# Optimization experiments

Measured on AMD Instinct MI355X. Metric: run time of the kernel, lower is better.

## Reference

```python
import jax, jax.numpy as jnp
import numpy as np

N = 100000   # num nodes
E = 3200000  # num edges (avg degree 32)
D = 256      # in_channels
H = 256      # hidden_dim
C = 1        # num_class
G = 512      # num graphs in batch


def setup_inputs() -> dict:
    key = jax.random.key(0)
    k = jax.random.split(key, 5)
    x = jax.random.normal(k[0], (N, D), dtype=jnp.float32)
    edge_index = jax.random.randint(k[1], (2, E), 0, N, dtype=jnp.int64)
    batch = jnp.sort(jax.random.randint(k[2], (N,), 0, G, dtype=jnp.int64))
    # GCNLayer.proj: Linear(D, H); model.lin: Linear(H, C)
    W1 = jax.random.normal(k[3], (H, D), dtype=jnp.float32) * 0.05
    b1 = jnp.zeros((H,), dtype=jnp.float32)
    W2 = jax.random.normal(k[4], (C, H), dtype=jnp.float32) * 0.05
    b2 = jnp.zeros((C,), dtype=jnp.float32)
    return {"x": x, "edge_index": edge_index, "batch": batch,
            "W1": W1, "b1": b1, "W2": W2, "b2": b2}


def reference(x, edge_index, batch, W1, b1, W2, b2):
    src, dst = edge_index[0], edge_index[1]
    # degree(edge_index[0]) over ORIGINAL edges (before self-loops), as in source
    deg = jnp.zeros((N,), x.dtype).at[src].add(jnp.asarray(1.0, x.dtype))
    norm = deg ** -0.5  # D^{-1/2}
    # (D^{-1/2} (A + I) D^{-1/2}) x
    # edge term: out[src] += norm[src] * norm[dst] * x[dst]
    msg = (norm[src] * norm[dst])[:, None] * x[dst]          # [E, D]
    agg = jax.ops.segment_sum(msg, src, num_segments=N)      # [N, D]
    agg = agg + (norm * norm)[:, None] * x                   # self-loop term
    h = jax.nn.relu(agg @ W1.T + b1)                          # [N, H]
    pooled = jax.ops.segment_max(h, batch, num_segments=G)   # [G, H]
    out = pooled @ W2.T + b2                                  # [G, 1]
    return jnp.squeeze(out, axis=1)                           # [G]
```

## Files before the change

kernel.cpp:

```cpp
#include <hip/hip_runtime.h>
#include <cstddef>

#define NN    100000
#define EE    3200000
#define GG    512
#define NBK2  391
#define BCAP  9216
#define TT    4096

typedef __attribute__((ext_vector_type(8))) short bf16x8;
typedef __attribute__((ext_vector_type(4))) float f32x4;
typedef __attribute__((ext_vector_type(8))) unsigned short u16x8;

struct U12 { unsigned a, b, c; };

static __device__ __forceinline__ unsigned short f2b(float f) {
  unsigned u = __float_as_uint(f);
  unsigned r = u + 0x7fffu + ((u >> 16) & 1u);
  return (unsigned short)(r >> 16);
}

__global__ __launch_bounds__(1024, 2) void k_split(const int* __restrict__ src,
                                                   const int* __restrict__ dst,
                                                   int* __restrict__ gcur,
                                                   int* __restrict__ pk) {
  __shared__ int hist[NBK2], st[NBK2], cur[NBK2], gbase[NBK2];
  __shared__ int sc[512];
  __shared__ int sorted[TT];
  __shared__ unsigned short binof[TT];
  const int tid = threadIdx.x;
  const int t0  = blockIdx.x * TT;
  const int tc  = min(TT, EE - t0);

  if (tid < NBK2) hist[tid] = 0;
  __syncthreads();
  int myk[4], myw[4];
#pragma unroll
  for (int r = 0; r < 4; ++r) {
    int j = r * 1024 + tid;
    myk[r] = -1;
    if (j < tc) {
      int s = src[t0 + j], d = dst[t0 + j];
      myk[r] = s >> 8;
      myw[r] = ((s & 255) << 17) | d;
      atomicAdd(&hist[myk[r]], 1);
    }
  }
  __syncthreads();
  if (tid < 512) sc[tid] = (tid < NBK2) ? hist[tid] : 0;
  __syncthreads();
  for (int d = 1; d < 512; d <<= 1) {
    int v = (tid < 512 && tid >= d) ? sc[tid - d] : 0;
    __syncthreads();
    if (tid < 512) sc[tid] += v;
    __syncthreads();
  }
  if (tid < NBK2) { st[tid] = tid ? sc[tid - 1] : 0; cur[tid] = st[tid]; }
  __syncthreads();
#pragma unroll
  for (int r = 0; r < 4; ++r) {
    if (myk[r] >= 0) {
      int pos = atomicAdd(&cur[myk[r]], 1);
      sorted[pos] = myw[r];
      binof[pos] = (unsigned short)myk[r];
    }
  }
  __syncthreads();
  if (tid < NBK2) {
    int c = cur[tid] - st[tid];
    gbase[tid] = c ? atomicAdd(&gcur[tid], c) : 0;
  }
  __syncthreads();
  for (int j = tid; j < tc; j += 1024) {
    int k   = binof[j];
    int idx = gbase[k] + (j - st[k]);
    if (idx < BCAP) pk[(size_t)k * BCAP + idx] = sorted[j];
  }
}

__global__ __launch_bounds__(512) void k_prep(const int* __restrict__ gcur,
                                              const int* __restrict__ pk,
                                              const float* __restrict__ x,
                                              const float* __restrict__ w1,
                                              unsigned short* __restrict__ wbf,
                                              int* __restrict__ csr,
                                              int* __restrict__ ro,
                                              int* __restrict__ xm) {
  __shared__ int hist[256], start[257], cur[256], sc[256];
  __shared__ float red[8];
  const int tid = threadIdx.x;
  const int b   = blockIdx.x;
  const int n0  = b * 256;

  if (tid < 256) hist[tid] = 0;
  __syncthreads();
  const int szc = min(gcur[b], BCAP);
  const int* __restrict__ pb = pk + (size_t)b * BCAP;
  for (int j = tid; j < szc; j += 512)
    atomicAdd(&hist[pb[j] >> 17], 1);
  __syncthreads();
  if (tid < 256) sc[tid] = hist[tid];
  __syncthreads();
  for (int d = 1; d < 256; d <<= 1) {
    int v = (tid < 256 && tid >= d) ? sc[tid - d] : 0;
    __syncthreads();
    if (tid < 256) sc[tid] += v;
    __syncthreads();
  }
  if (tid < 256) { start[tid] = tid ? sc[tid - 1] : 0; cur[tid] = start[tid]; }
  __syncthreads();
  if (tid == 0) start[256] = sc[255];
  __syncthreads();
  for (int j = tid; j < szc; j += 512) {
    int w = pb[j];
    int pos = atomicAdd(&cur[w >> 17], 1);
    csr[(size_t)b * BCAP + pos] = w & 0x1FFFF;
  }
  if (tid < 257) ro[b * 257 + tid] = start[tid];
  __syncthreads();

  float tmax = 0.f;
  for (int it = 0; it < 32; ++it) {
    int idx = it * 512 + tid;
    int row = idx >> 6, c4 = idx & 63;
    int n = n0 + row;
    int deg = start[row + 1] - start[row];
    if (n < NN && deg > 0) {
      float nr = rsqrtf((float)deg);
      float4 v = ((const float4*)x)[(size_t)n * 64 + c4];
      float m = fmaxf(fmaxf(fabsf(v.x), fabsf(v.y)), fmaxf(fabsf(v.z), fabsf(v.w)));
      tmax = fmaxf(tmax, nr * m);
    }
  }
#pragma unroll
  for (int k = 1; k < 64; k <<= 1) tmax = fmaxf(tmax, __shfl_xor(tmax, k, 64));
  if ((tid & 63) == 0) red[tid >> 6] = tmax;
  __syncthreads();
  if (tid == 0) {
    float m = red[0];
#pragma unroll
    for (int w = 1; w < 8; ++w) m = fmaxf(m, red[w]);
    atomicMax(xm, __float_as_int(m));
  }

  if (b < 64 && tid < 256) {
    int i = b * 256 + tid;
    float4 v = ((const float4*)w1)[i];
    ushort4 o;
    o.x = f2b(v.x); o.y = f2b(v.y); o.z = f2b(v.z); o.w = f2b(v.w);
    ((ushort4*)wbf)[i] = o;
  }
}

__global__ __launch_bounds__(256) void k_pack(const float* __restrict__ x,
                                              const int* __restrict__ ro,
                                              const int* __restrict__ xm,
                                              unsigned* __restrict__ y12) {
  const int tid = threadIdx.x;
  const int row = blockIdx.x * 8 + (tid >> 5);
  const int l32 = tid & 31;
  const int bkt = row >> 8, r = row & 255;
  const int deg = ro[bkt * 257 + r + 1] - ro[bkt * 257 + r];
  const float nr  = rsqrtf((float)deg);
  const float s   = __int_as_float(*xm);
  const float inv = 2047.0f / s;

  float4 a = ((const float4*)x)[(size_t)row * 64 + l32 * 2];
  float4 b = ((const float4*)x)[(size_t)row * 64 + l32 * 2 + 1];
  int q[8];
  float v[8] = {a.x, a.y, a.z, a.w, b.x, b.y, b.z, b.w};
#pragma unroll
  for (int c = 0; c < 8; ++c) {
    int t = (int)rintf(nr * v[c] * inv) + 2048;
    q[c] = min(4095, max(0, t));
  }
  U12 o;
  o.a = (unsigned)q[0] | ((unsigned)q[1] << 12) | ((unsigned)(q[2] & 0xFF) << 24);
  o.b = ((unsigned)q[2] >> 8) | ((unsigned)q[3] << 4) | ((unsigned)q[4] << 16) |
        ((unsigned)(q[5] & 0xF) << 28);
  o.c = ((unsigned)q[5] >> 4) | ((unsigned)q[6] << 8) | ((unsigned)q[7] << 20);
  ((U12*)y12)[(size_t)row * 32 + l32] = o;
}

__global__ __launch_bounds__(512, 8) void k_fused4(const int* __restrict__ ro,
                                                   const int* __restrict__ csr,
                                                   const unsigned* __restrict__ y12,
                                                   const unsigned short* __restrict__ wbf,
                                                   const float* __restrict__ b1,
                                                   const int* __restrict__ batch,
                                                   const int* __restrict__ xm,
                                                   int* __restrict__ pooled) {
  __shared__ __align__(16) unsigned short As[16][264];
  __shared__ int rs[17];
  __shared__ int bg[16];
  const int tid  = threadIdx.x;
  const int n0   = blockIdx.x * 16;
  const int bkt  = blockIdx.x >> 4;
  const int br   = (blockIdx.x & 15) * 16;
  const int wave = tid >> 6;
  const int lane = tid & 63;

  if (tid < 17) rs[tid] = ro[bkt * 257 + br + tid];
  else if (tid >= 64 && tid < 80) bg[tid - 64] = batch[n0 + tid - 64];
  __syncthreads();

  const int half = lane >> 5, l32 = lane & 31;
  const int il   = wave * 2 + half;
  const int i    = n0 + il;
  const U12* __restrict__ yr = (const U12*)y12;
  const int* __restrict__ ce = csr + (size_t)bkt * BCAP;
  const float s = __int_as_float(*xm);

  int acc[8];
#pragma unroll
  for (int c = 0; c < 8; ++c) acc[c] = 0;
#define UNP(V) do { unsigned w0 = (V).a, w1 = (V).b, w2 = (V).c;                  \
    acc[0] += (int)(w0 & 0xFFFu);                                                 \
    acc[1] += (int)((w0 >> 12) & 0xFFFu);                                         \
    acc[2] += (int)((w0 >> 24) | ((w1 & 0xFu) << 8));                             \
    acc[3] += (int)((w1 >> 4) & 0xFFFu);                                          \
    acc[4] += (int)((w1 >> 16) & 0xFFFu);                                         \
    acc[5] += (int)((w1 >> 28) | ((w2 & 0xFFu) << 4));                            \
    acc[6] += (int)((w2 >> 8) & 0xFFFu);                                          \
    acc[7] += (int)(w2 >> 20); } while (0)

  U12 sv = yr[(size_t)i * 32 + l32];
  UNP(sv);

  int e = rs[il];
  const int e1 = rs[il + 1];
  const int cnt = e1 - e + 1;
  const float ni = rsqrtf((float)(e1 - e));
  for (; e + 8 <= e1; e += 8) {
    int d0 = ce[e],     d1 = ce[e + 1], d2 = ce[e + 2], d3 = ce[e + 3];
    int d4 = ce[e + 4], d5 = ce[e + 5], d6 = ce[e + 6], d7 = ce[e + 7];
    U12 v0 = yr[(size_t)d0 * 32 + l32];
    U12 v1 = yr[(size_t)d1 * 32 + l32];
    U12 v2 = yr[(size_t)d2 * 32 + l32];
    U12 v3 = yr[(size_t)d3 * 32 + l32];
    U12 v4 = yr[(size_t)d4 * 32 + l32];
    U12 v5 = yr[(size_t)d5 * 32 + l32];
    U12 v6 = yr[(size_t)d6 * 32 + l32];
    U12 v7 = yr[(size_t)d7 * 32 + l32];
    UNP(v0); UNP(v1); UNP(v2); UNP(v3); UNP(v4); UNP(v5); UNP(v6); UNP(v7);
  }
  for (; e + 4 <= e1; e += 4) {
    int d0 = ce[e], d1 = ce[e + 1], d2 = ce[e + 2], d3 = ce[e + 3];
    U12 v0 = yr[(size_t)d0 * 32 + l32];
    U12 v1 = yr[(size_t)d1 * 32 + l32];
    U12 v2 = yr[(size_t)d2 * 32 + l32];
    U12 v3 = yr[(size_t)d3 * 32 + l32];
    UNP(v0); UNP(v1); UNP(v2); UNP(v3);
  }
  for (; e < e1; ++e) {
    U12 v = yr[(size_t)ce[e] * 32 + l32];
    UNP(v);
  }
#undef UNP
  const float fsc = ni * s * (1.0f / 2047.0f);
  const float boff = 2048.0f * (float)cnt;
  u16x8 o;
#pragma unroll
  for (int c = 0; c < 8; ++c) o[c] = f2b(fsc * ((float)acc[c] - boff));
  *(u16x8*)&As[il][l32 * 8] = o;
  __syncthreads();

  const int r16 = lane & 15, quad = lane >> 4;
  f32x4 acc4[2];
#pragma unroll
  for (int t = 0; t < 2; ++t) acc4[t] = (f32x4){0.f, 0.f, 0.f, 0.f};
  for (int kc = 0; kc < 8; ++kc) {
    bf16x8 af = *(const bf16x8*)&As[r16][kc * 32 + quad * 8];
#pragma unroll
    for (int ct = 0; ct < 2; ++ct) {
      const int n = wave * 32 + ct * 16 + r16;
      bf16x8 bf = *(const bf16x8*)(wbf + (size_t)n * 256 + kc * 32 + quad * 8);
      acc4[ct] = __builtin_amdgcn_mfma_f32_16x16x32_bf16(af, bf, acc4[ct], 0, 0, 0);
    }
  }

  const int g0 = bg[0], g15 = bg[15];
  if (g0 == g15) {
#pragma unroll
    for (int ct = 0; ct < 2; ++ct) {
      const int col = wave * 32 + ct * 16 + r16;
      const float bias = b1[col];
      float m = 0.f;
#pragma unroll
      for (int r = 0; r < 4; ++r) m = fmaxf(m, acc4[ct][r] + bias);
      m = fmaxf(m, __shfl_xor(m, 16, 64));
      m = fmaxf(m, __shfl_xor(m, 32, 64));
      if (quad == 0) atomicMax(&pooled[g0 * 256 + col], __float_as_int(m));
    }
  } else {
#pragma unroll
    for (int ct = 0; ct < 2; ++ct) {
      const int col = wave * 32 + ct * 16 + r16;
      const float bias = b1[col];
      for (int g = g0; g <= g15; ++g) {
        float m = 0.f;
#pragma unroll
        for (int r = 0; r < 4; ++r) {
          const int row = quad * 4 + r;
          float v = fmaxf(acc4[ct][r] + bias, 0.f);
          if (bg[row] == g) m = fmaxf(m, v);
        }
        m = fmaxf(m, __shfl_xor(m, 16, 64));
        m = fmaxf(m, __shfl_xor(m, 32, 64));
        if (quad == 0) atomicMax(&pooled[g * 256 + col], __float_as_int(m));
      }
    }
  }
}

__global__ void k_out(const float* __restrict__ pooled, const float* __restrict__ w2,
                      const float* __restrict__ b2, float* __restrict__ out) {
  const int wave = threadIdx.x >> 6;
  const int lane = threadIdx.x & 63;
  const int g = blockIdx.x * 4 + wave;
  float4 p = ((const float4*)pooled)[g * 64 + lane];
  float4 w = ((const float4*)w2)[lane];
  float s = p.x * w.x + p.y * w.y + p.z * w.z + p.w * w.w;
  for (int off = 32; off; off >>= 1) s += __shfl_down(s, off, 64);
  if (lane == 0) out[g] = s + b2[0];
}

extern "C" void kernel_launch(void* const* d_in, const int* in_sizes, int n_in,
                              void* d_out, int out_size, void* d_ws, size_t ws_size,
                              hipStream_t stream) {
  const float* x     = (const float*)d_in[0];
  const int*   ei    = (const int*)d_in[1];
  const int*   batch = (const int*)d_in[2];
  const float* W1    = (const float*)d_in[3];
  const float* b1    = (const float*)d_in[4];
  const float* W2    = (const float*)d_in[5];
  const float* b2    = (const float*)d_in[6];
  const int* src = ei;
  const int* dst = ei + EE;
  float* out = (float*)d_out;

  size_t off = 0;
  auto carve = [&](size_t bytes) -> void* {
    void* p = (char*)d_ws + off;
    off += (bytes + 255) & ~(size_t)255;
    return p;
  };
  int*   pooled = (int*)carve((size_t)GG * 256 * 4);
  int*   gcur   = (int*)carve((size_t)NBK2 * 4);
  int*   xm     = (int*)carve(4);
  const size_t zlen = off;
  unsigned* y12 = (unsigned*)carve((size_t)NN * 96 * 4);
  int*   pk     = (int*)carve((size_t)NBK2 * BCAP * 4);
  int*   csr    = (int*)carve((size_t)NBK2 * BCAP * 4);
  int*   ro     = (int*)carve((size_t)NBK2 * 257 * 4);
  unsigned short* wbf = (unsigned short*)carve(256 * 256 * 2);

  hipMemsetAsync(pooled, 0, zlen, stream);

  k_split<<<(EE + TT - 1) / TT, 1024, 0, stream>>>(src, dst, gcur, pk);
  k_prep <<<NBK2,               512,  0, stream>>>(gcur, pk, x, W1, wbf, csr, ro, xm);
  k_pack <<<NN / 8,             256,  0, stream>>>(x, ro, xm, y12);
  k_fused4<<<NN / 16,           512,  0, stream>>>(ro, csr, y12, wbf, b1, batch, xm, pooled);
  k_out  <<<GG / 4,             256,  0, stream>>>((const float*)pooled, W2, b2, out);
}
```

Measured before the change: 441.9 us.

## Move degree count and per-row abs-max into split kernel, simplify prep

k_split now also computes per-node degree with global atomics and a per-row absolute max of x (782 blocks × 128 rows covers all nodes). k_prep no longer builds a histogram from the packed buckets or rescans x. It takes the prefix sum from the degree array and reduces rsqrt(deg)*rowmax. k_pack reads degree directly. This removes a pass over the bucketed edges and a full read of x in k_prep, at the cost of 3.2M global atomics on deg and extra x reads inside k_split.

```diff
diff --git a/kernel.cpp b/kernel.cpp
--- a/kernel.cpp
+++ b/kernel.cpp
@@ -22,6 +22,9 @@
 
 __global__ __launch_bounds__(1024, 2) void k_split(const int* __restrict__ src,
                                                    const int* __restrict__ dst,
+                                                   const float* __restrict__ x,
+                                                   int* __restrict__ deg,
+                                                   float* __restrict__ rmax,
                                                    int* __restrict__ gcur,
                                                    int* __restrict__ pk) {
   __shared__ int hist[NBK2], st[NBK2], cur[NBK2], gbase[NBK2];
@@ -32,6 +35,20 @@
   const int t0  = blockIdx.x * TT;
   const int tc  = min(TT, EE - t0);
 
+  const int r0 = blockIdx.x * 128;
+  for (int it = 0; it < 8; ++it) {
+    int idx = it * 1024 + tid;
+    int row = r0 + (idx >> 6), c4 = idx & 63;
+    float m = 0.f;
+    if (row < NN) {
+      float4 v = ((const float4*)x)[(size_t)row * 64 + c4];
+      m = fmaxf(fmaxf(fabsf(v.x), fabsf(v.y)), fmaxf(fabsf(v.z), fabsf(v.w)));
+    }
+#pragma unroll
+    for (int k = 1; k < 64; k <<= 1) m = fmaxf(m, __shfl_xor(m, k, 64));
+    if ((tid & 63) == 0 && row < NN) rmax[row] = m;
+  }
+
   if (tid < NBK2) hist[tid] = 0;
   __syncthreads();
   int myk[4], myw[4];
@@ -44,6 +61,7 @@
       myk[r] = s >> 8;
       myw[r] = ((s & 255) << 17) | d;
       atomicAdd(&hist[myk[r]], 1);
+      atomicAdd(&deg[s], 1);
     }
   }
   __syncthreads();
@@ -80,26 +98,25 @@
 
 __global__ __launch_bounds__(512) void k_prep(const int* __restrict__ gcur,
                                               const int* __restrict__ pk,
-                                              const float* __restrict__ x,
+                                              const int* __restrict__ deg,
+                                              const float* __restrict__ rmax,
                                               const float* __restrict__ w1,
                                               unsigned short* __restrict__ wbf,
                                               int* __restrict__ csr,
                                               int* __restrict__ ro,
                                               int* __restrict__ xm) {
-  __shared__ int hist[256], start[257], cur[256], sc[256];
+  __shared__ int start[257], cur[256], sc[256];
   __shared__ float red[8];
   const int tid = threadIdx.x;
   const int b   = blockIdx.x;
   const int n0  = b * 256;
 
-  if (tid < 256) hist[tid] = 0;
-  __syncthreads();
-  const int szc = min(gcur[b], BCAP);
-  const int* __restrict__ pb = pk + (size_t)b * BCAP;
-  for (int j = tid; j < szc; j += 512)
-    atomicAdd(&hist[pb[j] >> 17], 1);
-  __syncthreads();
-  if (tid < 256) sc[tid] = hist[tid];
+  int dg = 0;
+  if (tid < 256) {
+    int n = n0 + tid;
+    dg = (n < NN) ? deg[n] : 0;
+    sc[tid] = dg;
+  }
   __syncthreads();
   for (int d = 1; d < 256; d <<= 1) {
     int v = (tid < 256 && tid >= d) ? sc[tid - d] : 0;
@@ -111,27 +128,18 @@
   __syncthreads();
   if (tid == 0) start[256] = sc[255];
   __syncthreads();
+  const int szc = min(gcur[b], BCAP);
+  const int* __restrict__ pb = pk + (size_t)b * BCAP;
   for (int j = tid; j < szc; j += 512) {
     int w = pb[j];
     int pos = atomicAdd(&cur[w >> 17], 1);
     csr[(size_t)b * BCAP + pos] = w & 0x1FFFF;
   }
   if (tid < 257) ro[b * 257 + tid] = start[tid];
-  __syncthreads();
 
   float tmax = 0.f;
-  for (int it = 0; it < 32; ++it) {
-    int idx = it * 512 + tid;
-    int row = idx >> 6, c4 = idx & 63;
-    int n = n0 + row;
-    int deg = start[row + 1] - start[row];
-    if (n < NN && deg > 0) {
-      float nr = rsqrtf((float)deg);
-      float4 v = ((const float4*)x)[(size_t)n * 64 + c4];
-      float m = fmaxf(fmaxf(fabsf(v.x), fabsf(v.y)), fmaxf(fabsf(v.z), fabsf(v.w)));
-      tmax = fmaxf(tmax, nr * m);
-    }
-  }
+  if (tid < 256 && n0 + tid < NN && dg > 0)
+    tmax = rsqrtf((float)dg) * rmax[n0 + tid];
 #pragma unroll
   for (int k = 1; k < 64; k <<= 1) tmax = fmaxf(tmax, __shfl_xor(tmax, k, 64));
   if ((tid & 63) == 0) red[tid >> 6] = tmax;
@@ -153,15 +161,13 @@
 }
 
 __global__ __launch_bounds__(256) void k_pack(const float* __restrict__ x,
-                                              const int* __restrict__ ro,
+                                              const int* __restrict__ deg,
                                               const int* __restrict__ xm,
                                               unsigned* __restrict__ y12) {
   const int tid = threadIdx.x;
   const int row = blockIdx.x * 8 + (tid >> 5);
   const int l32 = tid & 31;
-  const int bkt = row >> 8, r = row & 255;
-  const int deg = ro[bkt * 257 + r + 1] - ro[bkt * 257 + r];
-  const float nr  = rsqrtf((float)deg);
+  const float nr  = rsqrtf((float)deg[row]);
   const float s   = __int_as_float(*xm);
   const float inv = 2047.0f / s;
 
@@ -348,18 +354,20 @@
   int*   pooled = (int*)carve((size_t)GG * 256 * 4);
   int*   gcur   = (int*)carve((size_t)NBK2 * 4);
   int*   xm     = (int*)carve(4);
+  int*   deg    = (int*)carve((size_t)NN * 4);
   const size_t zlen = off;
   unsigned* y12 = (unsigned*)carve((size_t)NN * 96 * 4);
   int*   pk     = (int*)carve((size_t)NBK2 * BCAP * 4);
   int*   csr    = (int*)carve((size_t)NBK2 * BCAP * 4);
   int*   ro     = (int*)carve((size_t)NBK2 * 257 * 4);
+  float* rmax   = (float*)carve((size_t)NN * 4);
   unsigned short* wbf = (unsigned short*)carve(256 * 256 * 2);
 
   hipMemsetAsync(pooled, 0, zlen, stream);
 
-  k_split<<<(EE + TT - 1) / TT, 1024, 0, stream>>>(src, dst, gcur, pk);
-  k_prep <<<NBK2,               512,  0, stream>>>(gcur, pk, x, W1, wbf, csr, ro, xm);
-  k_pack <<<NN / 8,             256,  0, stream>>>(x, ro, xm, y12);
+  k_split<<<(EE + TT - 1) / TT, 1024, 0, stream>>>(src, dst, x, deg, rmax, gcur, pk);
+  k_prep <<<NBK2,               512,  0, stream>>>(gcur, pk, deg, rmax, W1, wbf, csr, ro, xm);
+  k_pack <<<NN / 8,             256,  0, stream>>>(x, deg, xm, y12);
   k_fused4<<<NN / 16,           512,  0, stream>>>(ro, csr, y12, wbf, b1, batch, xm, pooled);
   k_out  <<<GG / 4,             256,  0, stream>>>((const float*)pooled, W2, b2, out);
 }
```

New measurement: 544.2 us. +23.2%, slower.
